# Performance work log

Measured on AMD Instinct MI355X. Metric: run time of the kernel, lower is better.

The kernel has to match this reference:

```python
import jax, jax.numpy as jnp
import numpy as np

K = 16
SIGMA_ONE = 0.02
EXP_RANGE = 10.0
T_MIN = 1e-6


def setup_inputs() -> dict:
    key = jax.random.key(0)
    ks = jax.random.split(key, 6)
    B, D, H = 32, 49152, 16
    return {
        "mu": jax.random.normal(ks[0], (B, D), dtype=jnp.float32),
        "t": jax.random.uniform(ks[1], (B, 1), dtype=jnp.float32),
        "W1": jax.random.normal(ks[2], (2, H), dtype=jnp.float32) * 0.5,
        "b1": jax.random.normal(ks[3], (H,), dtype=jnp.float32) * 0.1,
        "W2": jax.random.normal(ks[4], (H, 2), dtype=jnp.float32) * 0.1,
        "b2": jax.random.normal(ks[5], (2,), dtype=jnp.float32) * 0.1,
    }


def reference(mu, t, W1, b1, W2, b2):
    # bin geometry: centers (2K-1)/K - 1 for K=1..k, lower/upper = center -/+ 1/k
    k_idx = jnp.arange(1, K + 1, dtype=mu.dtype)
    k_centers = (2.0 * k_idx - 1.0) / K - 1.0          # [K]
    k_lower = k_centers - 1.0 / K
    k_upper = k_centers + 1.0 / K

    gamma = 1.0 - jnp.power(jnp.asarray(SIGMA_ONE, mu.dtype), 2.0 * t)  # [B,1]

    # inner model: pointwise MLP on stacked (mu, t) -> (mean_eps, log_var_eps)
    x = jnp.stack([mu, jnp.broadcast_to(t, mu.shape)], axis=-1)  # [B,D,2]
    h = jax.nn.gelu(x @ W1 + b1)                                 # [B,D,H]
    out = h @ W2 + b2                                            # [B,D,2]
    mu_eps, ln_sigma_eps = out[..., 0], out[..., 1]

    var_scale = jnp.sqrt((1.0 - gamma) / gamma)                  # [B,1]
    mu_x = mu / gamma - var_scale * mu_eps                       # [B,D]
    sigma_x = jnp.maximum(
        var_scale * jnp.exp(jnp.clip(ln_sigma_eps, -EXP_RANGE, EXP_RANGE)),
        SIGMA_ONE,
    )
    cond = t < T_MIN                                             # [B,1]
    mu_x = jnp.where(cond, 0.0, mu_x)
    sigma_x = jnp.where(cond, 1.0, sigma_x)

    inv = (1.0 / (sigma_x * jnp.sqrt(jnp.asarray(2.0, mu.dtype))))[..., None]  # [B,D,1]
    mu_b = mu_x[..., None]                                       # [B,D,1]

    def normal_cdf(bins):  # bins [K] -> [B,D,K]
        return 0.5 * (1.0 + jax.lax.erf((bins - mu_b) * inv))

    cdf_lower = jnp.where(k_lower <= -1.0, 0.0, normal_cdf(k_lower))
    cdf_upper = jnp.where(k_upper >= 1.0, 1.0, normal_cdf(k_upper))
    return cdf_upper - cdf_lower                                 # [B,D,K]
```

## Files before the change

kernel.cpp:

```cpp
#include <hip/hip_runtime.h>
#include <math.h>

#define KBINS 16
#define HID 16

#define LN_SIGMA1 (-3.912023005428146f)

__global__ __launch_bounds__(256) void bfn_kernel(
    const float* __restrict__ mu,
    const float* __restrict__ t,
    const float* __restrict__ W1,
    const float* __restrict__ b1,
    const float* __restrict__ W2,
    const float* __restrict__ b2,
    float* __restrict__ out,
    int D)
{
    const int b = blockIdx.y;
    const int d = blockIdx.x * blockDim.x + threadIdx.x;
    if (d >= D) return;

    const float tb = t[b];
    const float e2t   = expf(2.0f * tb * LN_SIGMA1);
    const float gamma = -expm1f(2.0f * tb * LN_SIGMA1);
    const float inv_gamma = 1.0f / gamma;
    const float var_scale = sqrtf(e2t / gamma);
    const bool  tiny_t = (tb < 1e-6f);

    float w1a[HID], c1[HID], w20[HID], w21[HID];
#pragma unroll
    for (int i = 0; i < HID; ++i) {
        w1a[i] = W1[i];
        c1[i]  = fmaf(tb, W1[HID + i], b1[i]);
        w20[i] = W2[2 * i];
        w21[i] = W2[2 * i + 1];
    }
    const float bias0 = b2[0], bias1 = b2[1];

    const float m = mu[(size_t)b * D + d];

    float o0 = bias0, o1 = bias1;
#pragma unroll
    for (int i = 0; i < HID; ++i) {
        float pre = fmaf(m, w1a[i], c1[i]);
        float u = 0.7978845608028654f * fmaf(0.044715f * pre, pre * pre, pre);
        float th = 1.0f - 2.0f / (__expf(2.0f * u) + 1.0f);
        float h = 0.5f * pre * (1.0f + th);
        o0 = fmaf(h, w20[i], o0);
        o1 = fmaf(h, w21[i], o1);
    }

    float mu_x = fmaf(m, inv_gamma, -var_scale * o0);
    float lse = fminf(fmaxf(o1, -10.0f), 10.0f);
    float sigma_x = fmaxf(var_scale * __expf(lse), 0.02f);
    if (tiny_t) { mu_x = 0.0f; sigma_x = 1.0f; }

    const float inv = 0.70710678118654752f / sigma_x;

    float cdf[KBINS + 1];
    cdf[0] = 0.0f;
    cdf[KBINS] = 1.0f;
#pragma unroll
    for (int j = 1; j < KBINS; ++j) {
        float bj = (float)j * 0.125f - 1.0f;
        cdf[j] = 0.5f * (1.0f + erff((bj - mu_x) * inv));
    }

    float res[KBINS];
#pragma unroll
    for (int k = 0; k < KBINS; ++k) res[k] = cdf[k + 1] - cdf[k];

    float4* op = (float4*)(out + ((size_t)b * D + d) * KBINS);
#pragma unroll
    for (int q = 0; q < 4; ++q) {
        op[q] = make_float4(res[4 * q], res[4 * q + 1], res[4 * q + 2], res[4 * q + 3]);
    }
}

extern "C" void kernel_launch(void* const* d_in, const int* in_sizes, int n_in,
                              void* d_out, int out_size, void* d_ws, size_t ws_size,
                              hipStream_t stream) {
    const float* mu = (const float*)d_in[0];
    const float* t  = (const float*)d_in[1];
    const float* W1 = (const float*)d_in[2];
    const float* b1 = (const float*)d_in[3];
    const float* W2 = (const float*)d_in[4];
    const float* b2 = (const float*)d_in[5];
    float* out = (float*)d_out;

    const int B = in_sizes[1];
    const int D = in_sizes[0] / B;

    dim3 block(256);
    dim3 grid((D + 255) / 256, B);
    bfn_kernel<<<grid, block, 0, stream>>>(mu, t, W1, b1, W2, b2, out, D);
}
```

Baseline: 145.0 us.

## Stage outputs through LDS for coalesced stores and use cheaper GELU/erf approximations

Each thread now writes its 16 bin probabilities to padded shared memory, and the block then stores them as contiguous float4 lines to get fully coalesced global writes. GELU is rewritten as a sigmoid form with one exp and a hardware reciprocal. erf is replaced by an Abramowitz-Stegun style rational approximation. Uniform weights are moved into scalar registers and occupancy hints are added. The erf approximation has an error near 5e-4, which may exceed tolerance, and the LDS staging adds a barrier.

```diff
diff --git a/kernel.cpp b/kernel.cpp
--- a/kernel.cpp
+++ b/kernel.cpp
@@ -3,10 +3,13 @@
 
 #define KBINS 16
 #define HID 16
-
 #define LN_SIGMA1 (-3.912023005428146f)
 
-__global__ __launch_bounds__(256) void bfn_kernel(
+__device__ __forceinline__ float to_sgpr(float x) {
+    return __int_as_float(__builtin_amdgcn_readfirstlane(__float_as_int(x)));
+}
+
+__global__ __launch_bounds__(256, 4) void bfn_kernel(
     const float* __restrict__ mu,
     const float* __restrict__ t,
     const float* __restrict__ W1,
@@ -16,64 +19,93 @@
     float* __restrict__ out,
     int D)
 {
-    const int b = blockIdx.y;
-    const int d = blockIdx.x * blockDim.x + threadIdx.x;
-    if (d >= D) return;
+    __shared__ float lds[256 * 20];
 
-    const float tb = t[b];
-    const float e2t   = expf(2.0f * tb * LN_SIGMA1);
+    const int b   = blockIdx.y;
+    const int tid = threadIdx.x;
+    const int d0  = blockIdx.x * 256;
+    const int d   = d0 + tid;
+    const bool valid = (d < D);
+
+    const float tb    = t[b];
     const float gamma = -expm1f(2.0f * tb * LN_SIGMA1);
+    const float e2t   = 1.0f - gamma;
     const float inv_gamma = 1.0f / gamma;
-    const float var_scale = sqrtf(e2t / gamma);
+    const float var_scale = sqrtf(e2t * inv_gamma);
     const bool  tiny_t = (tb < 1e-6f);
 
     float w1a[HID], c1[HID], w20[HID], w21[HID];
 #pragma unroll
     for (int i = 0; i < HID; ++i) {
-        w1a[i] = W1[i];
+        w1a[i] = to_sgpr(W1[i]);
         c1[i]  = fmaf(tb, W1[HID + i], b1[i]);
-        w20[i] = W2[2 * i];
-        w21[i] = W2[2 * i + 1];
+        w20[i] = to_sgpr(W2[2 * i]);
+        w21[i] = to_sgpr(W2[2 * i + 1]);
     }
-    const float bias0 = b2[0], bias1 = b2[1];
+    const float bias0 = to_sgpr(b2[0]);
+    const float bias1 = to_sgpr(b2[1]);
 
-    const float m = mu[(size_t)b * D + d];
+    const float m = valid ? mu[(size_t)b * D + d] : 0.0f;
 
     float o0 = bias0, o1 = bias1;
 #pragma unroll
     for (int i = 0; i < HID; ++i) {
         float pre = fmaf(m, w1a[i], c1[i]);
-        float u = 0.7978845608028654f * fmaf(0.044715f * pre, pre * pre, pre);
-        float th = 1.0f - 2.0f / (__expf(2.0f * u) + 1.0f);
-        float h = 0.5f * pre * (1.0f + th);
+        float p2  = pre * pre;
+        float z   = pre * fmaf(p2, -0.0713552235f, -1.5957691216f);
+        float e   = __expf(z);
+        float h   = pre * __builtin_amdgcn_rcpf(1.0f + e);
         o0 = fmaf(h, w20[i], o0);
         o1 = fmaf(h, w21[i], o1);
     }
 
     float mu_x = fmaf(m, inv_gamma, -var_scale * o0);
-    float lse = fminf(fmaxf(o1, -10.0f), 10.0f);
+    float lse  = fminf(fmaxf(o1, -10.0f), 10.0f);
     float sigma_x = fmaxf(var_scale * __expf(lse), 0.02f);
     if (tiny_t) { mu_x = 0.0f; sigma_x = 1.0f; }
 
-    const float inv = 0.70710678118654752f / sigma_x;
+    const float inv = 0.70710678118f * __builtin_amdgcn_rcpf(sigma_x);
+    const float x0  = (-0.875f - mu_x) * inv;
+    const float stp = 0.125f * inv;
 
     float cdf[KBINS + 1];
-    cdf[0] = 0.0f;
-    cdf[KBINS] = 1.0f;
+    cdf[0] = 0.0f; cdf[KBINS] = 1.0f;
 #pragma unroll
     for (int j = 1; j < KBINS; ++j) {
-        float bj = (float)j * 0.125f - 1.0f;
-        cdf[j] = 0.5f * (1.0f + erff((bj - mu_x) * inv));
+        float x  = fmaf((float)(j - 1), stp, x0);
+        float ax = fabsf(x);
+        float p  = fmaf(0.078108f, ax, 0.000972f);
+        p        = fmaf(p, ax, 0.230389f);
+        p        = fmaf(p, ax, 0.278393f);
+        float q  = fmaf(p, ax, 1.0f);
+        float q2 = q * q;
+        float q4 = q2 * q2;
+        float hr = 0.5f * __builtin_amdgcn_rcpf(q4);
+        cdf[j] = (x >= 0.0f) ? (1.0f - hr) : hr;
     }
 
-    float res[KBINS];
+    const bool full = (d0 + 256 <= D);
+    if (full) {
+        float4* row = (float4*)(lds + tid * 20);
 #pragma unroll
-    for (int k = 0; k < KBINS; ++k) res[k] = cdf[k + 1] - cdf[k];
-
-    float4* op = (float4*)(out + ((size_t)b * D + d) * KBINS);
+        for (int s = 0; s < 4; ++s)
+            row[s] = make_float4(cdf[4*s+1] - cdf[4*s],   cdf[4*s+2] - cdf[4*s+1],
+                                 cdf[4*s+3] - cdf[4*s+2], cdf[4*s+4] - cdf[4*s+3]);
+        __syncthreads();
+        float4* og = (float4*)out + ((size_t)b * D + d0) * 4;
 #pragma unroll
-    for (int q = 0; q < 4; ++q) {
-        op[q] = make_float4(res[4 * q], res[4 * q + 1], res[4 * q + 2], res[4 * q + 3]);
+        for (int s = 0; s < 4; ++s) {
+            int f = s * 256 + tid;
+            int e = f >> 2;
+            int c = (f & 3) << 2;
+            og[f] = *(const float4*)(lds + e * 20 + c);
+        }
+    } else if (valid) {
+        float4* op = (float4*)(out + ((size_t)b * D + d) * (size_t)KBINS);
+#pragma unroll
+        for (int s = 0; s < 4; ++s)
+            op[s] = make_float4(cdf[4*s+1] - cdf[4*s],   cdf[4*s+2] - cdf[4*s+1],
+                                 cdf[4*s+3] - cdf[4*s+2], cdf[4*s+4] - cdf[4*s+3]);
     }
 }
 
```

New measurement: 125.8 us. 13.3% less time.
